# Optimization experiments

Hardware: AMD Instinct MI355X
Metric: run time of the kernel (lower is better)

## Reference

```python
import jax, jax.numpy as jnp
import numpy as np

Q = 4096   # query_size = argument_size*relation_size*position_size = 32*16*8
L = 8192   # number of context rows


def setup_inputs() -> dict:
    key = jax.random.key(0)
    k1, k2, k3 = jax.random.split(key, 3)
    query = jax.random.normal(k1, (Q,), dtype=jnp.float32)
    context_vector = jax.random.normal(k2, (L, Q), dtype=jnp.float32)
    # torch Linear(2Q, Q, bias=False): weight shape [Q, 2Q], scaled init
    K_w = jax.random.normal(k3, (Q, 2 * Q), dtype=jnp.float32) / np.sqrt(2 * Q)
    return {"query": query, "context_vector": context_vector, "K_w": K_w}


def reference(query, context_vector, K_w):
    # score[l] = <context_vector[l], query>  -> [L]
    score = context_vector @ query
    attention = jax.nn.softmax(score, axis=0)          # softmax over L
    s_t = attention @ context_vector                    # [Q]
    gamma = jnp.concatenate([query, s_t])               # [2Q]
    return K_w @ gamma                                   # Linear(2Q -> Q), no bias
```

## Files before the change

kernel.cpp:

```cpp
#include <hip/hip_runtime.h>

#define Q 4096
#define L 8192
#define NCB 2048
#define RPB 4
#define NKB 1024

__device__ __forceinline__ void ld_g2l16(const float* gp, float* lp) {
    __builtin_amdgcn_global_load_lds(
        (const __attribute__((address_space(1))) void*)gp,
        (__attribute__((address_space(3))) void*)lp,
        16, 0, 0);
}

__global__ __launch_bounds__(256) void k1_kernel(
    const float* __restrict__ qvec, const float* __restrict__ ctx,
    const float* __restrict__ Kw, float* __restrict__ partial,
    float* __restrict__ score, float* __restrict__ out1)
{
    __shared__ float rows[RPB * Q];
    __shared__ float sc[RPB];
    const int tid  = threadIdx.x;
    const int lane = tid & 63;
    const int wid  = tid >> 6;

    if (blockIdx.x < NCB) {
        const float* gbase = ctx + (size_t)blockIdx.x * RPB * Q;
        #pragma unroll
        for (int k = 0; k < 16; ++k) {
            const int idx4 = tid + k * 256;
            ld_g2l16(gbase + (size_t)idx4 * 4, rows + (size_t)idx4 * 4);
        }
        __syncthreads();

        {
            const float4* __restrict__ rl = (const float4*)(rows) + wid * (Q / 4);
            const float4* __restrict__ qg = (const float4*)qvec;
            float a0 = 0.f, a1 = 0.f;
            #pragma unroll
            for (int c = 0; c < 16; c += 2) {
                float4 x0 = rl[(c + 0) * 64 + lane], y0 = qg[(c + 0) * 64 + lane];
                float4 x1 = rl[(c + 1) * 64 + lane], y1 = qg[(c + 1) * 64 + lane];
                a0 = fmaf(x0.x, y0.x, a0); a0 = fmaf(x0.y, y0.y, a0);
                a0 = fmaf(x0.z, y0.z, a0); a0 = fmaf(x0.w, y0.w, a0);
                a1 = fmaf(x1.x, y1.x, a1); a1 = fmaf(x1.y, y1.y, a1);
                a1 = fmaf(x1.z, y1.z, a1); a1 = fmaf(x1.w, y1.w, a1);
            }
            float d = a0 + a1;
            #pragma unroll
            for (int off = 32; off > 0; off >>= 1) d += __shfl_down(d, off, 64);
            if (lane == 0) {
                sc[wid] = d;
                score[blockIdx.x * RPB + wid] = d;
            }
        }
        __syncthreads();

        const float s0 = sc[0], s1 = sc[1], s2 = sc[2], s3 = sc[3];
        const float mb = fmaxf(fmaxf(s0, s1), fmaxf(s2, s3));
        const float w0 = __expf(s0 - mb), w1 = __expf(s1 - mb);
        const float w2 = __expf(s2 - mb), w3 = __expf(s3 - mb);

        const float4* __restrict__ r4 = (const float4*)rows;
        float4* __restrict__ pb = (float4*)(partial + (size_t)blockIdx.x * Q);
        #pragma unroll
        for (int k = 0; k < 4; ++k) {
            const int c4 = tid + k * 256;
            float4 v0 = r4[c4];
            float4 v1 = r4[1024 + c4];
            float4 v2 = r4[2048 + c4];
            float4 v3 = r4[3072 + c4];
            float4 a;
            a.x = fmaf(w3, v3.x, fmaf(w2, v2.x, fmaf(w1, v1.x, w0 * v0.x)));
            a.y = fmaf(w3, v3.y, fmaf(w2, v2.y, fmaf(w1, v1.y, w0 * v0.y)));
            a.z = fmaf(w3, v3.z, fmaf(w2, v2.z, fmaf(w1, v1.z, w0 * v0.z)));
            a.w = fmaf(w3, v3.w, fmaf(w2, v2.w, fmaf(w1, v1.w, w0 * v0.w)));
            pb[c4] = a;
        }
    } else {
        const int i = (blockIdx.x - NCB) * 4 + wid;
        const float4* __restrict__ row = (const float4*)(Kw + (size_t)i * (2 * Q));
        const float4* __restrict__ qg  = (const float4*)qvec;
        float a0 = 0.f, a1 = 0.f, a2 = 0.f, a3 = 0.f;
        #pragma unroll
        for (int c = 0; c < 16; c += 4) {
            float4 x0 = row[(c + 0) * 64 + lane], y0 = qg[(c + 0) * 64 + lane];
            float4 x1 = row[(c + 1) * 64 + lane], y1 = qg[(c + 1) * 64 + lane];
            float4 x2 = row[(c + 2) * 64 + lane], y2 = qg[(c + 2) * 64 + lane];
            float4 x3 = row[(c + 3) * 64 + lane], y3 = qg[(c + 3) * 64 + lane];
            a0 = fmaf(x0.x, y0.x, a0); a0 = fmaf(x0.y, y0.y, a0);
            a0 = fmaf(x0.z, y0.z, a0); a0 = fmaf(x0.w, y0.w, a0);
            a1 = fmaf(x1.x, y1.x, a1); a1 = fmaf(x1.y, y1.y, a1);
            a1 = fmaf(x1.z, y1.z, a1); a1 = fmaf(x1.w, y1.w, a1);
            a2 = fmaf(x2.x, y2.x, a2); a2 = fmaf(x2.y, y2.y, a2);
            a2 = fmaf(x2.z, y2.z, a2); a2 = fmaf(x2.w, y2.w, a2);
            a3 = fmaf(x3.x, y3.x, a3); a3 = fmaf(x3.y, y3.y, a3);
            a3 = fmaf(x3.z, y3.z, a3); a3 = fmaf(x3.w, y3.w, a3);
        }
        float d = (a0 + a1) + (a2 + a3);
        #pragma unroll
        for (int off = 32; off > 0; off >>= 1) d += __shfl_down(d, off, 64);
        if (lane == 0) out1[i] = d;
    }
}

__global__ __launch_bounds__(256) void k2_kernel(
    const float* __restrict__ partial, const float* __restrict__ score,
    float* __restrict__ s_t)
{
    __shared__ float wb[NCB];
    __shared__ float red[4];
    __shared__ float4 sacc[64][4];
    const int tid  = threadIdx.x;
    const int lane = tid & 63;
    const int wid  = tid >> 6;

    float lm = -3.4e38f;
    for (int i = tid; i < L; i += 256) lm = fmaxf(lm, score[i]);
    #pragma unroll
    for (int off = 32; off > 0; off >>= 1) lm = fmaxf(lm, __shfl_down(lm, off, 64));
    if (lane == 0) red[wid] = lm;
    __syncthreads();
    const float M = fmaxf(fmaxf(red[0], red[1]), fmaxf(red[2], red[3]));
    __syncthreads();

    float lz = 0.f;
    for (int i = tid; i < L; i += 256) lz += __expf(score[i] - M);
    #pragma unroll
    for (int off = 32; off > 0; off >>= 1) lz += __shfl_down(lz, off, 64);
    if (lane == 0) red[wid] = lz;
    __syncthreads();
    const float invZ = 1.f / (red[0] + red[1] + red[2] + red[3]);

    for (int b = tid; b < NCB; b += 256) {
        const float4 s4 = ((const float4*)score)[b];
        const float mb = fmaxf(fmaxf(s4.x, s4.y), fmaxf(s4.z, s4.w));
        wb[b] = __expf(mb - M);
    }
    __syncthreads();

    const int c  = tid & 3;
    const int g  = tid >> 2;
    const int c4 = blockIdx.x * 4 + c;
    const float4* __restrict__ p = (const float4*)partial;
    float4 acc = make_float4(0.f, 0.f, 0.f, 0.f);
    for (int b = g; b < NCB; b += 64) {
        const float w = wb[b];
        float4 v = p[(size_t)b * (Q / 4) + c4];
        acc.x = fmaf(w, v.x, acc.x); acc.y = fmaf(w, v.y, acc.y);
        acc.z = fmaf(w, v.z, acc.z); acc.w = fmaf(w, v.w, acc.w);
    }
    sacc[g][c] = acc;
    __syncthreads();
    if (g == 0) {
        float4 t = sacc[0][c];
        #pragma unroll
        for (int gg = 1; gg < 64; ++gg) {
            float4 u = sacc[gg][c];
            t.x += u.x; t.y += u.y; t.z += u.z; t.w += u.w;
        }
        t.x *= invZ; t.y *= invZ; t.z *= invZ; t.w *= invZ;
        ((float4*)s_t)[c4] = t;
    }
}

__global__ __launch_bounds__(256) void k3_kernel(
    const float* __restrict__ Kw, const float* __restrict__ s_t,
    const float* __restrict__ out1, float* __restrict__ out)
{
    const int lane = threadIdx.x & 63;
    const int wid  = threadIdx.x >> 6;
    const int i = blockIdx.x * 4 + wid;
    const float4* __restrict__ row = (const float4*)(Kw + (size_t)i * (2 * Q) + Q);
    const float4* __restrict__ sg  = (const float4*)s_t;
    float a0 = 0.f, a1 = 0.f, a2 = 0.f, a3 = 0.f;
    #pragma unroll
    for (int c = 0; c < 16; c += 4) {
        float4 x0 = row[(c + 0) * 64 + lane], y0 = sg[(c + 0) * 64 + lane];
        float4 x1 = row[(c + 1) * 64 + lane], y1 = sg[(c + 1) * 64 + lane];
        float4 x2 = row[(c + 2) * 64 + lane], y2 = sg[(c + 2) * 64 + lane];
        float4 x3 = row[(c + 3) * 64 + lane], y3 = sg[(c + 3) * 64 + lane];
        a0 = fmaf(x0.x, y0.x, a0); a0 = fmaf(x0.y, y0.y, a0);
        a0 = fmaf(x0.z, y0.z, a0); a0 = fmaf(x0.w, y0.w, a0);
        a1 = fmaf(x1.x, y1.x, a1); a1 = fmaf(x1.y, y1.y, a1);
        a1 = fmaf(x1.z, y1.z, a1); a1 = fmaf(x1.w, y1.w, a1);
        a2 = fmaf(x2.x, y2.x, a2); a2 = fmaf(x2.y, y2.y, a2);
        a2 = fmaf(x2.z, y2.z, a2); a2 = fmaf(x2.w, y2.w, a2);
        a3 = fmaf(x3.x, y3.x, a3); a3 = fmaf(x3.y, y3.y, a3);
        a3 = fmaf(x3.z, y3.z, a3); a3 = fmaf(x3.w, y3.w, a3);
    }
    float d = (a0 + a1) + (a2 + a3);
    #pragma unroll
    for (int off = 32; off > 0; off >>= 1) d += __shfl_down(d, off, 64);
    if (lane == 0) out[i] = out1[i] + d;
}

extern "C" void kernel_launch(void* const* d_in, const int* in_sizes, int n_in,
                              void* d_out, int out_size, void* d_ws, size_t ws_size,
                              hipStream_t stream)
{
    const float* query = (const float*)d_in[0];
    const float* ctx   = (const float*)d_in[1];
    const float* Kw    = (const float*)d_in[2];
    float* out = (float*)d_out;

    float* ws      = (float*)d_ws;
    float* score   = ws;
    float* out1    = ws + L;
    float* s_t     = ws + L + Q;
    float* partial = ws + L + 2 * Q;

    k1_kernel<<<NCB + NKB, 256, 0, stream>>>(query, ctx, Kw, partial, score, out1);
    k2_kernel<<<Q / 4 / 4, 256, 0, stream>>>(partial, score, s_t);
    k3_kernel<<<Q / 4, 256, 0, stream>>>(Kw, s_t, out1, out);
}
```

Measured before the change: 77.75 us.

## Drop LDS staging in context pass and process eight rows per block

The context pass no longer stages rows into LDS with direct global-to-LDS loads. Each thread keeps its slice of the query in registers and computes partial dots for 8 rows, which a cross-wave reduction combines. It then re-reads the same rows from global memory (expected to hit cache) to form the weighted partial sum. This halves the number of partial vectors and blocks that the second kernel must reduce, and the second kernel's thread mapping is adjusted to match. The trade is a second global read of each context row in exchange for no LDS footprint, which allows higher occupancy.

```diff
diff --git a/kernel.cpp b/kernel.cpp
--- a/kernel.cpp
+++ b/kernel.cpp
@@ -2,81 +2,82 @@
 
 #define Q 4096
 #define L 8192
-#define NCB 2048
-#define RPB 4
-#define NKB 1024
-
-__device__ __forceinline__ void ld_g2l16(const float* gp, float* lp) {
-    __builtin_amdgcn_global_load_lds(
-        (const __attribute__((address_space(1))) void*)gp,
-        (__attribute__((address_space(3))) void*)lp,
-        16, 0, 0);
-}
+#define RPB 8
+#define NCB (L / RPB)
+#define NKW 1024
 
 __global__ __launch_bounds__(256) void k1_kernel(
     const float* __restrict__ qvec, const float* __restrict__ ctx,
     const float* __restrict__ Kw, float* __restrict__ partial,
     float* __restrict__ score, float* __restrict__ out1)
 {
-    __shared__ float rows[RPB * Q];
-    __shared__ float sc[RPB];
+    __shared__ float sred[4][RPB];
     const int tid  = threadIdx.x;
     const int lane = tid & 63;
     const int wid  = tid >> 6;
 
     if (blockIdx.x < NCB) {
-        const float* gbase = ctx + (size_t)blockIdx.x * RPB * Q;
-        #pragma unroll
-        for (int k = 0; k < 16; ++k) {
-            const int idx4 = tid + k * 256;
-            ld_g2l16(gbase + (size_t)idx4 * 4, rows + (size_t)idx4 * 4);
+        const float4* __restrict__ qg = (const float4*)qvec;
+        const float4* __restrict__ cb = (const float4*)ctx;
+        const int r0 = blockIdx.x * RPB;
+
+        float4 qr[4];
+        #pragma unroll
+        for (int k = 0; k < 4; ++k) qr[k] = qg[tid + k * 256];
+
+        float d[RPB];
+        #pragma unroll
+        for (int r = 0; r < RPB; ++r) {
+            float a = 0.f;
+            #pragma unroll
+            for (int k = 0; k < 4; ++k) {
+                float4 v = cb[(size_t)(r0 + r) * (Q / 4) + tid + k * 256];
+                a = fmaf(v.x, qr[k].x, a); a = fmaf(v.y, qr[k].y, a);
+                a = fmaf(v.z, qr[k].z, a); a = fmaf(v.w, qr[k].w, a);
+            }
+            d[r] = a;
+        }
+        #pragma unroll
+        for (int r = 0; r < RPB; ++r) {
+            float a = d[r];
+            #pragma unroll
+            for (int off = 32; off > 0; off >>= 1) a += __shfl_down(a, off, 64);
+            if (lane == 0) sred[wid][r] = a;
         }
         __syncthreads();
 
-        {
-            const float4* __restrict__ rl = (const float4*)(rows) + wid * (Q / 4);
-            const float4* __restrict__ qg = (const float4*)qvec;
-            float a0 = 0.f, a1 = 0.f;
+        float s[RPB], mb = -3.4e38f;
+        #pragma unroll
+        for (int r = 0; r < RPB; ++r) {
+            s[r] = sred[0][r] + sred[1][r] + sred[2][r] + sred[3][r];
+            mb = fmaxf(mb, s[r]);
+        }
+        float w[RPB];
+        #pragma unroll
+        for (int r = 0; r < RPB; ++r) w[r] = __expf(s[r] - mb);
+        if (tid < RPB) {
+            score[r0 + tid] = sred[0][tid] + sred[1][tid] +
+                              sred[2][tid] + sred[3][tid];
+        }
+
+        float4 acc[4];
+        #pragma unroll
+        for (int k = 0; k < 4; ++k) acc[k] = make_float4(0.f, 0.f, 0.f, 0.f);
+        #pragma unroll
+        for (int r = 0; r < RPB; ++r) {
+            const float wr = w[r];
             #pragma unroll
-            for (int c = 0; c < 16; c += 2) {
-                float4 x0 = rl[(c + 0) * 64 + lane], y0 = qg[(c + 0) * 64 + lane];
-                float4 x1 = rl[(c + 1) * 64 + lane], y1 = qg[(c + 1) * 64 + lane];
-                a0 = fmaf(x0.x, y0.x, a0); a0 = fmaf(x0.y, y0.y, a0);
-                a0 = fmaf(x0.z, y0.z, a0); a0 = fmaf(x0.w, y0.w, a0);
-                a1 = fmaf(x1.x, y1.x, a1); a1 = fmaf(x1.y, y1.y, a1);
-                a1 = fmaf(x1.z, y1.z, a1); a1 = fmaf(x1.w, y1.w, a1);
+            for (int k = 0; k < 4; ++k) {
+                float4 v = cb[(size_t)(r0 + r) * (Q / 4) + tid + k * 256];
+                acc[k].x = fmaf(wr, v.x, acc[k].x);
+                acc[k].y = fmaf(wr, v.y, acc[k].y);
+                acc[k].z = fmaf(wr, v.z, acc[k].z);
+                acc[k].w = fmaf(wr, v.w, acc[k].w);
             }
-            float d = a0 + a1;
-            #pragma unroll
-            for (int off = 32; off > 0; off >>= 1) d += __shfl_down(d, off, 64);
-            if (lane == 0) {
-                sc[wid] = d;
-                score[blockIdx.x * RPB + wid] = d;
-            }
-        }
-        __syncthreads();
-
-        const float s0 = sc[0], s1 = sc[1], s2 = sc[2], s3 = sc[3];
-        const float mb = fmaxf(fmaxf(s0, s1), fmaxf(s2, s3));
-        const float w0 = __expf(s0 - mb), w1 = __expf(s1 - mb);
-        const float w2 = __expf(s2 - mb), w3 = __expf(s3 - mb);
-
-        const float4* __restrict__ r4 = (const float4*)rows;
+        }
         float4* __restrict__ pb = (float4*)(partial + (size_t)blockIdx.x * Q);
         #pragma unroll
-        for (int k = 0; k < 4; ++k) {
-            const int c4 = tid + k * 256;
-            float4 v0 = r4[c4];
-            float4 v1 = r4[1024 + c4];
-            float4 v2 = r4[2048 + c4];
-            float4 v3 = r4[3072 + c4];
-            float4 a;
-            a.x = fmaf(w3, v3.x, fmaf(w2, v2.x, fmaf(w1, v1.x, w0 * v0.x)));
-            a.y = fmaf(w3, v3.y, fmaf(w2, v2.y, fmaf(w1, v1.y, w0 * v0.y)));
-            a.z = fmaf(w3, v3.z, fmaf(w2, v2.z, fmaf(w1, v1.z, w0 * v0.z)));
-            a.w = fmaf(w3, v3.w, fmaf(w2, v2.w, fmaf(w1, v1.w, w0 * v0.w)));
-            pb[c4] = a;
-        }
+        for (int k = 0; k < 4; ++k) pb[tid + k * 256] = acc[k];
     } else {
         const int i = (blockIdx.x - NCB) * 4 + wid;
         const float4* __restrict__ row = (const float4*)(Kw + (size_t)i * (2 * Q));
@@ -97,10 +98,10 @@
             a3 = fmaf(x3.x, y3.x, a3); a3 = fmaf(x3.y, y3.y, a3);
             a3 = fmaf(x3.z, y3.z, a3); a3 = fmaf(x3.w, y3.w, a3);
         }
-        float d = (a0 + a1) + (a2 + a3);
-        #pragma unroll
-        for (int off = 32; off > 0; off >>= 1) d += __shfl_down(d, off, 64);
-        if (lane == 0) out1[i] = d;
+        float dd = (a0 + a1) + (a2 + a3);
+        #pragma unroll
+        for (int off = 32; off > 0; off >>= 1) dd += __shfl_down(dd, off, 64);
+        if (lane == 0) out1[i] = dd;
     }
 }
 
@@ -110,7 +111,7 @@
 {
     __shared__ float wb[NCB];
     __shared__ float red[4];
-    __shared__ float4 sacc[64][4];
+    __shared__ float4 sacc[32][8];
     const int tid  = threadIdx.x;
     const int lane = tid & 63;
     const int wid  = tid >> 6;
@@ -133,18 +134,20 @@
     const float invZ = 1.f / (red[0] + red[1] + red[2] + red[3]);
 
     for (int b = tid; b < NCB; b += 256) {
-        const float4 s4 = ((const float4*)score)[b];
-        const float mb = fmaxf(fmaxf(s4.x, s4.y), fmaxf(s4.z, s4.w));
-        wb[b] = __expf(mb - M);
-    }
-    __syncthreads();
-
-    const int c  = tid & 3;
-    const int g  = tid >> 2;
-    const int c4 = blockIdx.x * 4 + c;
+        const float4 sa = ((const float4*)score)[2 * b];
+        const float4 sb = ((const float4*)score)[2 * b + 1];
+        float m8 = fmaxf(fmaxf(fmaxf(sa.x, sa.y), fmaxf(sa.z, sa.w)),
+                         fmaxf(fmaxf(sb.x, sb.y), fmaxf(sb.z, sb.w)));
+        wb[b] = __expf(m8 - M);
+    }
+    __syncthreads();
+
+    const int c  = tid & 7;
+    const int g  = tid >> 3;
+    const int c4 = blockIdx.x * 8 + c;
     const float4* __restrict__ p = (const float4*)partial;
     float4 acc = make_float4(0.f, 0.f, 0.f, 0.f);
-    for (int b = g; b < NCB; b += 64) {
+    for (int b = g; b < NCB; b += 32) {
         const float w = wb[b];
         float4 v = p[(size_t)b * (Q / 4) + c4];
         acc.x = fmaf(w, v.x, acc.x); acc.y = fmaf(w, v.y, acc.y);
@@ -155,7 +158,7 @@
     if (g == 0) {
         float4 t = sacc[0][c];
         #pragma unroll
-        for (int gg = 1; gg < 64; ++gg) {
+        for (int gg = 1; gg < 32; ++gg) {
             float4 u = sacc[gg][c];
             t.x += u.x; t.y += u.y; t.z += u.z; t.w += u.w;
         }
@@ -189,10 +192,10 @@
         a3 = fmaf(x3.x, y3.x, a3); a3 = fmaf(x3.y, y3.y, a3);
         a3 = fmaf(x3.z, y3.z, a3); a3 = fmaf(x3.w, y3.w, a3);
     }
-    float d = (a0 + a1) + (a2 + a3);
-    #pragma unroll
-    for (int off = 32; off > 0; off >>= 1) d += __shfl_down(d, off, 64);
-    if (lane == 0) out[i] = out1[i] + d;
+    float dd = (a0 + a1) + (a2 + a3);
+    #pragma unroll
+    for (int off = 32; off > 0; off >>= 1) dd += __shfl_down(dd, off, 64);
+    if (lane == 0) out[i] = out1[i] + dd;
 }
 
 extern "C" void kernel_launch(void* const* d_in, const int* in_sizes, int n_in,
@@ -210,7 +213,7 @@
     float* s_t     = ws + L + Q;
     float* partial = ws + L + 2 * Q;
 
-    k1_kernel<<<NCB + NKB, 256, 0, stream>>>(query, ctx, Kw, partial, score, out1);
-    k2_kernel<<<Q / 4 / 4, 256, 0, stream>>>(partial, score, s_t);
+    k1_kernel<<<NCB + NKW, 256, 0, stream>>>(query, ctx, Kw, partial, score, out1);
+    k2_kernel<<<Q / 4 / 8, 256, 0, stream>>>(partial, score, s_t);
     k3_kernel<<<Q / 4, 256, 0, stream>>>(Kw, s_t, out1, out);
 }
```

Measured after the change: 85.07 us. 9.4% more time.
